# Optimization experiments

Hardware: AMD Instinct MI355X
Metric: run time of the kernel (lower is better)

The kernel has to match this reference:

```python
import jax, jax.numpy as jnp
import numpy as np
from jax.tree_util import tree_map

B, T, D = 2, 4096, 1024
C = 512            # chunk_size
P = 16             # n_persistent
H = 2048           # neural-memory hidden
FFN = 4 * D        # ffn_mult * d_model
LR, BETA, ALPHA = 0.01, 0.9, 0.01   # memory lr / momentum / decay
EPS_LN = 1e-5


def _l2norm(x):
    n = jnp.sqrt(jnp.sum(x * x, axis=-1, keepdims=True))
    return x / jnp.maximum(n, 1e-12)


def _ln(x, g, b):
    m = jnp.mean(x, axis=-1, keepdims=True)
    v = jnp.mean((x - m) ** 2, axis=-1, keepdims=True)
    return (x - m) * jax.lax.rsqrt(v + EPS_LN) * g + b


def _mem_mlp(mem, x):
    h = jax.nn.silu(x @ mem['w0'] + mem['b0'])
    return h @ mem['w1'] + mem['b1']


def setup_inputs() -> dict:
    key = jax.random.key(0)
    ks = iter(jax.random.split(key, 32))
    w = lambda *s: jax.random.normal(next(ks), s, jnp.float32) * 0.02
    return dict(
        x=jax.random.normal(next(ks), (B, T, D), jnp.float32),
        wq_ctx=w(D, D), wq=w(D, D), wk=w(D, D), wv=w(D, D),
        w_attn_out=w(D, D), w_gate=w(D, D),
        gate_g=jnp.ones(D), gate_b=jnp.zeros(D),
        n1_g=jnp.ones(D), n1_b=jnp.zeros(D),
        n2_g=jnp.ones(D), n2_b=jnp.zeros(D),
        ffn_w1=w(D, FFN), ffn_b1=jnp.zeros(FFN),
        ffn_w2=w(FFN, D), ffn_b2=jnp.zeros(D),
        pers=w(P, D),
        mem_w0=w(D, H), mem_b0=jnp.zeros(H),
        mem_w1=w(H, D), mem_b1=jnp.zeros(D),
        mem_wk=w(D, D), mem_wv=w(D, D),
    )


def reference(x, wq_ctx, wq, wk, wv, w_attn_out, w_gate, gate_g, gate_b,
              n1_g, n1_b, n2_g, n2_b, ffn_w1, ffn_b1, ffn_w2, ffn_b2,
              pers, mem_w0, mem_b0, mem_w1, mem_b1, mem_wk, mem_wv):
    Bv, Tv, Dv = x.shape
    n_chunks = Tv // C
    scale = Dv ** 0.5
    S = P + 2 * C   # persistent + retrieved-memory tokens + segment
    # prefix-aware causal mask: i attends to j if j < P (persistent prefix) or j <= i
    ii = jnp.arange(S)[:, None]
    jj = jnp.arange(S)[None, :]
    mask = (jj < P) | (jj <= ii)                      # (S, S)

    mem0 = dict(w0=mem_w0, b0=mem_b0, w1=mem_w1, b1=mem_b1)
    mom0 = tree_map(jnp.zeros_like, mem0)

    def attn(seq):                                    # cosine causal attention, single head
        q = _l2norm(seq @ wq) * scale
        k = _l2norm(seq @ wk)
        v = seq @ wv
        scores = jnp.einsum('bqd,bkd->bqk', q, k)
        scores = jnp.where(mask, scores, -jnp.inf)
        a = jax.nn.softmax(scores, axis=-1)
        return jnp.einsum('bqk,bkd->bqd', a, v) @ w_attn_out

    def step(carry, seg):                             # seg: (B, C, D)
        mem, mom = carry
        h = _mem_mlp(mem, _l2norm(seg @ wq_ctx))      # memory retrieval, (B, C, D)
        aug = jnp.concatenate(
            [jnp.broadcast_to(pers, (Bv, P, Dv)), h, seg], axis=1)  # (B, S, D)
        y_aug = aug + attn(_ln(aug, n1_g, n1_b))
        y_t = y_aug[:, P + C:, :]                     # strip persistent, keep last C

        # surprise-gradient memory update with momentum + decay
        kk = y_t @ mem_wk
        vv = y_t @ mem_wv
        loss = lambda m: 0.5 * jnp.sum((_mem_mlp(m, kk) - vv) ** 2) / (Bv * C)
        g = jax.grad(loss)(mem)
        mom = tree_map(lambda m_, g_: BETA * m_ + g_, mom, g)
        mem = tree_map(lambda p_, m_: (1.0 - ALPHA) * p_ - LR * m_, mem, mom)

        mem_out = _mem_mlp(mem, _l2norm(y_t @ wq_ctx))
        gate = jax.nn.sigmoid(_ln(y_t, gate_g, gate_b) @ w_gate)
        o = y_t * gate + mem_out * (1.0 - gate)
        h2 = _ln(o, n2_g, n2_b)
        o = o + (jax.nn.silu(h2 @ ffn_w1 + ffn_b1) @ ffn_w2 + ffn_b2)
        return (mem, mom), o

    x_chunks = x.reshape(Bv, n_chunks, C, Dv).transpose(1, 0, 2, 3)
    _, outs = jax.lax.scan(step, (mem0, mom0), x_chunks)   # (n_chunks, B, C, D)
    return outs.transpose(1, 0, 2, 3).reshape(Bv, Tv, Dv)
```

## Files before the change

kernel.cpp:

```cpp
#include <hip/hip_runtime.h>

#define DD 1024
#define HH 2048
#define TT 4096
#define CC 512
#define PPc 16
#define SB 1040
#define KA 1088
#define FFd 4096
#define NCH 8

typedef _Float16 f16x8 __attribute__((ext_vector_type(8)));
typedef float f32x4 __attribute__((ext_vector_type(4)));

typedef const __attribute__((address_space(1))) _Float16* gas_t;
typedef __attribute__((address_space(3))) _Float16* las_t;

__device__ __forceinline__ void async_cp16(const _Float16* g, _Float16* l) {
    __builtin_amdgcn_global_load_lds((gas_t)g, (las_t)l, 16, 0, 0);
}

template<int N> __device__ __forceinline__ void waitvm() {
    static_assert(N == 0 || N == 2 || N == 3 || N == 4 || N == 6 || N == 8, "unsupported vmcnt");
    if constexpr (N == 0)      asm volatile("s_waitcnt vmcnt(0)" ::: "memory");
    else if constexpr (N == 2) asm volatile("s_waitcnt vmcnt(2)" ::: "memory");
    else if constexpr (N == 3) asm volatile("s_waitcnt vmcnt(3)" ::: "memory");
    else if constexpr (N == 4) asm volatile("s_waitcnt vmcnt(4)" ::: "memory");
    else if constexpr (N == 6) asm volatile("s_waitcnt vmcnt(6)" ::: "memory");
    else                       asm volatile("s_waitcnt vmcnt(8)" ::: "memory");
}
#define BARRIER() asm volatile("s_barrier" ::: "memory")

struct GP {
    const _Float16* A; long bsA;
    const _Float16* Bt; long bsB;
    const float* bias;
    const float* resid; long ldr, bsR;
    const float* aux;   long ldx, bsX;
    float* Cf; long ldc, bsC;
    _Float16* Ch; long ldh, bsH;
    _Float16* Ct; long ldt, bsT;
    float* Mom;
    float* Cf2;
    float s1, s2;
    int M, N, K, act;
};

template<int BM, int BN>
__global__ __launch_bounds__(256) void gemm16(GP g)
{
    constexpr int WM = BM / 2, WN = BN / 2;
    constexpr int FA = WM / 16, FB = WN / 16;
    constexpr int LA = BM / 64, LB = BN / 64;
    constexpr int LL = LA + LB;
    constexpr int APAN = BM * 32, BPAN = BN * 32;
    __shared__ _Float16 smem[4 * (APAN + BPAN)];
    const int tid = threadIdx.x;

    const int gx = gridDim.x, gy = gridDim.y;
    const int nwg = gx * gy * (int)gridDim.z;
    const int orig = ((int)blockIdx.z * gy + (int)blockIdx.y) * gx + (int)blockIdx.x;
    const int xcd = orig & 7, loc = orig >> 3;
    const int q8 = nwg >> 3, r8 = nwg & 7;
    const int lid = (xcd < r8 ? xcd * (q8 + 1) : r8 * (q8 + 1) + (xcd - r8) * q8) + loc;
    const int bxi = lid % gx;
    const int rem = lid / gx;
    const int byi = rem % gy;
    const int z = rem / gy;

    const int K = g.K;
    const int m0 = byi * BM, n0 = bxi * BN;
    const _Float16* Ab = g.A + (long)z * g.bsA + (long)m0 * K;
    const _Float16* Bb = g.Bt + (long)z * g.bsB + (long)n0 * K;
    const int wave = tid >> 6, lane = tid & 63;
    const int wr = wave >> 1, wc = wave & 1;
    const int fr = lane & 15, kq = lane >> 4;
    const int srow = tid >> 2;
    const int scol = (tid & 3) * 8;
    f32x4 acc[FA][FB] = {};

    auto stage = [&](int q, int kk) {
#pragma unroll
        for (int r = 0; r < LA; ++r)
            async_cp16(Ab + (long)(r * 64 + srow) * K + kk + scol,
                       &smem[q * APAN + r * 2048 + wave * 512]);
#pragma unroll
        for (int r = 0; r < LB; ++r)
            async_cp16(Bb + (long)(r * 64 + srow) * K + kk + scol,
                       &smem[4 * APAN + q * BPAN + r * 2048 + wave * 512]);
    };

    auto compute = [&](int q) {
        f16x8 af[FA], bf[FB];
        const int ab = q * APAN + (wr * WM + fr) * 32 + kq * 8;
#pragma unroll
        for (int i = 0; i < FA; ++i) af[i] = *(const f16x8*)&smem[ab + i * 512];
        const int bb = 4 * APAN + q * BPAN + (wc * WN + fr) * 32 + kq * 8;
#pragma unroll
        for (int j = 0; j < FB; ++j) bf[j] = *(const f16x8*)&smem[bb + j * 512];
#pragma unroll
        for (int i = 0; i < FA; ++i)
#pragma unroll
            for (int j = 0; j < FB; ++j)
                acc[i][j] = __builtin_amdgcn_mfma_f32_16x16x32_f16(af[i], bf[j], acc[i][j], 0, 0, 0);
    };

    const int nk = K >> 5;
    stage(0, 0); stage(1, 32); stage(2, 64);
    for (int t = 0; t < nk - 2; ++t) {
        waitvm<2 * LL>();
        BARRIER();
        if (t + 3 < nk) stage((t + 3) & 3, (t + 3) << 5);
        compute(t & 3);
    }
    waitvm<LL>(); BARRIER(); compute((nk - 2) & 3);
    waitvm<0>();  BARRIER(); compute((nk - 1) & 3);

#pragma unroll
    for (int i = 0; i < FA; ++i) {
        const int gm0 = m0 + wr * WM + i * 16 + kq * 4;
#pragma unroll
        for (int j = 0; j < FB; ++j) {
            const int gn = n0 + wc * WN + j * 16 + fr;
            if (gn >= g.N) continue;
            if (g.act == 3) {
#pragma unroll
                for (int r = 0; r < 4; ++r) {
                    const int gm = gm0 + r;
                    if (gm >= g.M) continue;
                    const long idx = (long)gm * g.ldc + gn;
                    const float m = 0.9f * g.Mom[idx] + acc[i][j][r];
                    g.Mom[idx] = m;
                    const float v = 0.99f * g.Cf[idx] - 0.01f * m;
                    g.Cf[idx] = v;
                    if (g.Ch) g.Ch[(long)gm * g.ldh + gn] = (_Float16)v;
                    acc[i][j][r] = v;
                }
            } else if (g.act == 4) {
                const int seg = gn >> 10, gl = gn & 1023;
#pragma unroll
                for (int r = 0; r < 4; ++r) {
                    const int gm = gm0 + r;
                    if (gm >= g.M) continue;
                    const float v = acc[i][j][r];
                    if (seg == 0) g.Ch[(long)gm * 1024 + gl] = (_Float16)v;
                    else if (seg == 1) g.Cf[(long)gm * 1024 + gl] = v;
                    else g.Cf2[(long)gm * 1024 + gl] = v;
                }
            } else {
                const float bv = g.bias ? g.bias[gn] : 0.f;
#pragma unroll
                for (int r = 0; r < 4; ++r) {
                    const int gm = gm0 + r;
                    if (gm >= g.M) continue;
                    const float raw = acc[i][j][r] + bv;
                    float av = raw;
                    if (g.act == 1) av = raw / (1.f + __expf(-raw));
                    else if (g.act == 2) {
                        const float a = g.aux[(long)z * g.bsX + (long)gm * g.ldx + gn];
                        const float s = 1.f / (1.f + __expf(-a));
                        av = raw * (s * (1.f + a * (1.f - s)));
                    }
                    float v = g.s1 * av;
                    if (g.resid) v += g.s2 * g.resid[(long)z * g.bsR + (long)gm * g.ldr + gn];
                    if (g.Cf) g.Cf[(long)z * g.bsC + (long)gm * g.ldc + gn] = (g.act == 1) ? raw : v;
                    if (g.Ch) g.Ch[(long)z * g.bsH + (long)gm * g.ldh + gn] = (_Float16)v;
                    acc[i][j][r] = v;
                }
            }
        }
    }

    if (g.Ct && (g.act != 4 || n0 < 1024)) {
        constexpr int TP = BM + 8;
        __syncthreads();
#pragma unroll
        for (int i = 0; i < FA; ++i) {
            const int lm = wr * WM + i * 16 + kq * 4;
#pragma unroll
            for (int j = 0; j < FB; ++j) {
                const int ln = wc * WN + j * 16 + fr;
#pragma unroll
                for (int r = 0; r < 4; ++r)
                    smem[ln * TP + lm + r] = (_Float16)acc[i][j][r];
            }
        }
        __syncthreads();
        constexpr int TPC = 256 / BN;
        constexpr int SEG = BM / TPC;
        const int ln = tid / TPC, part = tid % TPC;
        const int gn = n0 + ln;
        if (gn < g.N) {
            const int gmb = m0 + part * SEG;
            _Float16* dst = g.Ct + (long)z * g.bsT + (long)gn * g.ldt + gmb;
            const _Float16* src = &smem[ln * TP + part * SEG];
#pragma unroll
            for (int gi = 0; gi < SEG / 8; ++gi)
                if (gmb + gi * 8 < g.M)
                    *(uint4*)(dst + gi * 8) = *(const uint4*)(src + gi * 8);
        }
    }
}

__global__ void cvt_k(const float* __restrict__ in, _Float16* __restrict__ out, long n)
{
    long i = ((long)blockIdx.x * 256 + threadIdx.x) * 4;
    if (i >= n) return;
    const float4 v = *(const float4*)(in + i);
    out[i] = (_Float16)v.x; out[i + 1] = (_Float16)v.y;
    out[i + 2] = (_Float16)v.z; out[i + 3] = (_Float16)v.w;
}

__global__ void cvtT_k(const float* __restrict__ in, _Float16* __restrict__ out, int R, int C)
{
    __shared__ _Float16 t[64][65];
    const int c0 = blockIdx.x * 64, r0 = blockIdx.y * 64;
    const int tid = threadIdx.x;
    for (int i = 0; i < 16; ++i) {
        const int lin = i * 256 + tid;
        const int r = lin >> 6, cc = lin & 63;
        t[r][cc] = (_Float16)in[(long)(r0 + r) * C + c0 + cc];
    }
    __syncthreads();
    for (int i = 0; i < 16; ++i) {
        const int lin = i * 256 + tid;
        const int r2 = lin >> 6, c2 = lin & 63;
        out[(long)(c0 + r2) * R + r0 + c2] = t[c2][r2];
    }
}

__global__ void l2n16s_k(const float* __restrict__ in, long ld,
                         _Float16* __restrict__ out, float scale)
{
    const long row = blockIdx.x;
    const float* p = in + row * ld;
    _Float16* q = out + row * DD;
    const int t = threadIdx.x;
    float e0 = p[t], e1 = p[t + 256], e2 = p[t + 512], e3 = p[t + 768];
    __shared__ float rq[256];
    rq[t] = e0 * e0 + e1 * e1 + e2 * e2 + e3 * e3;
    __syncthreads();
    for (int k = 128; k; k >>= 1) { if (t < k) rq[t] += rq[t + k]; __syncthreads(); }
    const float f = scale / fmaxf(sqrtf(rq[0]), 1e-12f);
    q[t] = (_Float16)(e0 * f); q[t + 256] = (_Float16)(e1 * f);
    q[t + 512] = (_Float16)(e2 * f); q[t + 768] = (_Float16)(e3 * f);
}

__global__ void l2qk_k(const float* __restrict__ qk, _Float16* __restrict__ q16,
                       _Float16* __restrict__ k16)
{
    const int blk = blockIdx.x;
    const float* p; _Float16* o; float scale;
    if (blk < 1024) {
        const int b = blk >> 9, r = blk & 511;
        p = qk + (long)(b * SB + PPc + CC + r) * 2048;
        o = q16 + (long)blk * DD; scale = 32.f;
    } else {
        const int row = blk - 1024;
        p = qk + (long)row * 2048 + 1024;
        o = k16 + (long)row * DD; scale = 1.f;
    }
    const int t = threadIdx.x;
    float e0 = p[t], e1 = p[t + 256], e2 = p[t + 512], e3 = p[t + 768];
    __shared__ float rq[256];
    rq[t] = e0 * e0 + e1 * e1 + e2 * e2 + e3 * e3;
    __syncthreads();
    for (int k = 128; k; k >>= 1) { if (t < k) rq[t] += rq[t + k]; __syncthreads(); }
    const float f = scale / fmaxf(sqrtf(rq[0]), 1e-12f);
    o[t] = (_Float16)(e0 * f); o[t + 256] = (_Float16)(e1 * f);
    o[t + 512] = (_Float16)(e2 * f); o[t + 768] = (_Float16)(e3 * f);
}

__global__ void ln16_k(const float* __restrict__ x, const float* __restrict__ g,
                       const float* __restrict__ b, _Float16* __restrict__ o)
{
    const long row = blockIdx.x;
    const float* p = x + row * DD;
    _Float16* q = o + row * DD;
    const int t = threadIdx.x;
    float e0 = p[t], e1 = p[t + 256], e2 = p[t + 512], e3 = p[t + 768];
    __shared__ float rs[256], rq[256];
    rs[t] = e0 + e1 + e2 + e3;
    rq[t] = e0 * e0 + e1 * e1 + e2 * e2 + e3 * e3;
    __syncthreads();
    for (int k = 128; k; k >>= 1) {
        if (t < k) { rs[t] += rs[t + k]; rq[t] += rq[t + k]; }
        __syncthreads();
    }
    const float mean = rs[0] * (1.f / DD);
    const float inv = rsqrtf(rq[0] * (1.f / DD) - mean * mean + 1e-5f);
    q[t]       = (_Float16)((e0 - mean) * inv * g[t]       + b[t]);
    q[t + 256] = (_Float16)((e1 - mean) * inv * g[t + 256] + b[t + 256]);
    q[t + 512] = (_Float16)((e2 - mean) * inv * g[t + 512] + b[t + 512]);
    q[t + 768] = (_Float16)((e3 - mean) * inv * g[t + 768] + b[t + 768]);
}

__global__ void lnaug_k(const float* __restrict__ x, const float* __restrict__ pers,
                        const float* __restrict__ h, const float* __restrict__ g,
                        const float* __restrict__ b, _Float16* __restrict__ out, int c)
{
    const int row = blockIdx.x;
    const int bb = row / SB, i = row % SB;
    const float* p;
    if (i < PPc) p = pers + (long)i * DD;
    else if (i < PPc + CC) p = h + (long)(bb * CC + i - PPc) * DD;
    else p = x + (long)(bb * TT + c * CC + (i - PPc - CC)) * DD;
    _Float16* q = out + (long)row * DD;
    const int t = threadIdx.x;
    float e0 = p[t], e1 = p[t + 256], e2 = p[t + 512], e3 = p[t + 768];
    __shared__ float rs[256], rq[256];
    rs[t] = e0 + e1 + e2 + e3;
    rq[t] = e0 * e0 + e1 * e1 + e2 * e2 + e3 * e3;
    __syncthreads();
    for (int k = 128; k; k >>= 1) {
        if (t < k) { rs[t] += rs[t + k]; rq[t] += rq[t + k]; }
        __syncthreads();
    }
    const float mean = rs[0] * (1.f / DD);
    const float inv = rsqrtf(rq[0] * (1.f / DD) - mean * mean + 1e-5f);
    q[t]       = (_Float16)((e0 - mean) * inv * g[t]       + b[t]);
    q[t + 256] = (_Float16)((e1 - mean) * inv * g[t + 256] + b[t + 256]);
    q[t + 512] = (_Float16)((e2 - mean) * inv * g[t + 512] + b[t + 512]);
    q[t + 768] = (_Float16)((e3 - mean) * inv * g[t + 768] + b[t + 768]);
}

__global__ void softmax16_k(const float* __restrict__ sc, _Float16* __restrict__ pr)
{
    const int blk = blockIdx.x;
    const int r = blk & 511;
    const int i = PPc + CC + r;
    const float* p = sc + (long)blk * SB;
    _Float16* q = pr + (long)blk * KA;
    const int t = threadIdx.x;
    __shared__ float red[256];
    float mx = -3.0e38f;
    for (int j = t; j < SB; j += 256)
        if (j <= i) mx = fmaxf(mx, p[j]);
    red[t] = mx; __syncthreads();
    for (int k = 128; k; k >>= 1) { if (t < k) red[t] = fmaxf(red[t], red[t + k]); __syncthreads(); }
    mx = red[0]; __syncthreads();
    float sum = 0.f;
    for (int j = t; j < SB; j += 256)
        if (j <= i) sum += __expf(p[j] - mx);
    red[t] = sum; __syncthreads();
    for (int k = 128; k; k >>= 1) { if (t < k) red[t] += red[t + k]; __syncthreads(); }
    const float inv = 1.f / red[0];
    for (int j = t; j < KA; j += 256) {
        float e = 0.f;
        if (j < SB && j <= i) e = __expf(p[j] - mx) * inv;
        q[j] = (_Float16)e;
    }
}

__global__ void gateln2_k(const float* __restrict__ yt, const float* __restrict__ gp,
                          const float* __restrict__ mo, const float* __restrict__ g,
                          const float* __restrict__ b, float* __restrict__ OF,
                          _Float16* __restrict__ o16)
{
    const long row = blockIdx.x;
    const int t = threadIdx.x;
    float e[4];
    __shared__ float rs[256], rq[256];
    float ssum = 0.f, qsum = 0.f;
#pragma unroll
    for (int k = 0; k < 4; ++k) {
        const long idx = row * DD + t + k * 256;
        const float s = 1.f / (1.f + __expf(-gp[idx]));
        e[k] = yt[idx] * s + mo[idx] * (1.f - s);
        OF[idx] = e[k];
        ssum += e[k]; qsum += e[k] * e[k];
    }
    rs[t] = ssum; rq[t] = qsum;
    __syncthreads();
    for (int k = 128; k; k >>= 1) {
        if (t < k) { rs[t] += rs[t + k]; rq[t] += rq[t + k]; }
        __syncthreads();
    }
    const float mean = rs[0] * (1.f / DD);
    const float inv = rsqrtf(rq[0] * (1.f / DD) - mean * mean + 1e-5f);
#pragma unroll
    for (int k = 0; k < 4; ++k) {
        const int cc = t + k * 256;
        o16[row * DD + cc] = (_Float16)((e[k] - mean) * inv * g[cc] + b[cc]);
    }
}

__global__ void rowsum2_k(const _Float16* __restrict__ rT, const _Float16* __restrict__ daT,
                          float* __restrict__ db1, float* __restrict__ db0)
{
    const int blk = blockIdx.x;
    const _Float16* p; float* o;
    if (blk < 1024) { p = rT + (long)blk * 1024; o = db1 + blk; }
    else { p = daT + (long)(blk - 1024) * 1024; o = db0 + (blk - 1024); }
    const int t = threadIdx.x;
    __shared__ float red[256];
    red[t] = (float)p[t] + (float)p[t + 256] + (float)p[t + 512] + (float)p[t + 768];
    __syncthreads();
    for (int k = 128; k; k >>= 1) { if (t < k) red[t] += red[t + k]; __syncthreads(); }
    if (t == 0) *o = red[0];
}

__global__ void biasup_k(float* __restrict__ mb0, float* __restrict__ mob0,
                         const float* __restrict__ db0,
                         float* __restrict__ mb1, float* __restrict__ mob1,
                         const float* __restrict__ db1)
{
    const int i = blockIdx.x * 256 + threadIdx.x;
    if (i < HH) {
        const float m = 0.9f * mob0[i] + db0[i];
        mob0[i] = m;
        mb0[i] = 0.99f * mb0[i] - 0.01f * m;
    } else {
        const int j = i - HH;
        if (j < DD) {
            const float m = 0.9f * mob1[j] + db1[j];
            mob1[j] = m;
            mb1[j] = 0.99f * mb1[j] - 0.01f * m;
        }
    }
}

__global__ void zero_k(float* __restrict__ p, long n)
{
    long i = (long)blockIdx.x * 256 + threadIdx.x;
    const long st = (long)gridDim.x * 256;
    for (; i < n; i += st) p[i] = 0.f;
}

extern "C" void kernel_launch(void* const* d_in, const int* in_sizes, int n_in,
                              void* d_out, int out_size, void* d_ws, size_t ws_size,
                              hipStream_t stream)
{
    const float* x          = (const float*)d_in[0];
    const float* wq_ctx     = (const float*)d_in[1];
    const float* wq         = (const float*)d_in[2];
    const float* wk         = (const float*)d_in[3];
    const float* wv         = (const float*)d_in[4];
    const float* w_attn_out = (const float*)d_in[5];
    const float* w_gate     = (const float*)d_in[6];
    const float* gate_g     = (const float*)d_in[7];
    const float* gate_b     = (const float*)d_in[8];
    const float* n1_g       = (const float*)d_in[9];
    const float* n1_b       = (const float*)d_in[10];
    const float* n2_g       = (const float*)d_in[11];
    const float* n2_b       = (const float*)d_in[12];
    const float* ffn_w1     = (const float*)d_in[13];
    const float* ffn_b1     = (const float*)d_in[14];
    const float* ffn_w2     = (const float*)d_in[15];
    const float* ffn_b2     = (const float*)d_in[16];
    const float* pers       = (const float*)d_in[17];
    const float* mem_w0_in  = (const float*)d_in[18];
    const float* mem_b0_in  = (const float*)d_in[19];
    const float* mem_w1_in  = (const float*)d_in[20];
    const float* mem_b1_in  = (const float*)d_in[21];
    const float* mem_wk     = (const float*)d_in[22];
    const float* mem_wv     = (const float*)d_in[23];
    float* out = (float*)d_out;
    (void)in_sizes; (void)n_in; (void)out_size; (void)ws_size;

    char* cur = (char*)d_ws;
    auto allocF = [&](size_t n) { float* p = (float*)cur; cur += n * 4; return p; };
    auto allocH = [&](size_t n) { _Float16* p = (_Float16*)cur; cur += n * 2; return p; };

    float* mw0   = allocF((size_t)DD * HH);
    float* mw1   = allocF((size_t)HH * DD);
    float* mb0   = allocF(HH);
    float* mb1   = allocF(DD);
    float* mom   = allocF((size_t)DD * HH * 2 + HH + DD);
    float* mom_w0 = mom, *mom_w1 = mom + (size_t)DD * HH;
    float* mom_b0 = mom_w1 + (size_t)HH * DD, *mom_b1 = mom_b0 + HH;
    float* F32A  = allocF((size_t)1024 * DD);
    float* F32B  = allocF((size_t)1024 * DD);
    float* F32C  = allocF((size_t)1024 * HH);
    float* F32QK = allocF((size_t)2112 * 2048);
    float* YTF   = allocF((size_t)1024 * DD);
    float* OF    = allocF((size_t)1024 * DD);
    float* db0   = allocF(HH);
    float* db1   = allocF(DD);

    _Float16* x16    = allocH((size_t)2 * TT * DD);
    _Float16* wqcT   = allocH((size_t)DD * DD);
    _Float16* wqkT   = allocH((size_t)2048 * DD);
    _Float16* wvT    = allocH((size_t)DD * DD);
    _Float16* waoT   = allocH((size_t)DD * DD);
    _Float16* wgT    = allocH((size_t)DD * DD);
    _Float16* wmixT  = allocH((size_t)3072 * DD);
    _Float16* f1T    = allocH((size_t)FFd * DD);
    _Float16* f2T    = allocH((size_t)DD * FFd);
    _Float16* w0T    = allocH((size_t)HH * DD);
    _Float16* w1T    = allocH((size_t)DD * HH);
    _Float16* w1p    = allocH((size_t)HH * DD);
    _Float16* xn16   = allocH((size_t)1024 * DD);
    _Float16* h116   = allocH((size_t)1024 * HH);
    _Float16* laug16 = allocH((size_t)2208 * DD);
    _Float16* q16    = allocH((size_t)1024 * DD);
    _Float16* k16    = allocH((size_t)2208 * DD);
    _Float16* vT16   = allocH((size_t)2 * DD * KA);
    _Float16* pr16   = allocH((size_t)2 * 512 * KA);
    _Float16* ao16   = allocH((size_t)1024 * DD);
    _Float16* yt16   = allocH((size_t)1024 * DD);
    _Float16* kk16   = allocH((size_t)1024 * DD);
    _Float16* kkT16  = allocH((size_t)DD * 1024);
    _Float16* hs16   = allocH((size_t)1024 * HH);
    _Float16* hsT16  = allocH((size_t)HH * 1024);
    _Float16* r16    = allocH((size_t)1024 * DD);
    _Float16* rT16   = allocH((size_t)DD * 1024);
    _Float16* da0T   = allocH((size_t)HH * 1024);
    _Float16* qm16   = allocH((size_t)1024 * DD);
    _Float16* a216   = allocH((size_t)1024 * HH);
    _Float16* gl16   = allocH((size_t)1024 * DD);
    _Float16* h216   = allocH((size_t)1024 * DD);
    _Float16* f116   = allocH((size_t)1024 * FFd);

    auto launch = [&](int bm, int bn, int nz, const GP& g) {
        dim3 grid((g.N + bn - 1) / bn, (g.M + bm - 1) / bm, nz);
        if (bm == 128)     gemm16<128, 128><<<grid, 256, 0, stream>>>(g);
        else if (bn == 128) gemm16<64, 128><<<grid, 256, 0, stream>>>(g);
        else                gemm16<64, 64><<<grid, 256, 0, stream>>>(g);
    };

    hipMemcpyAsync(mw0, mem_w0_in, sizeof(float) * DD * HH, hipMemcpyDeviceToDevice, stream);
    hipMemcpyAsync(mw1, mem_w1_in, sizeof(float) * HH * DD, hipMemcpyDeviceToDevice, stream);
    hipMemcpyAsync(mb0, mem_b0_in, sizeof(float) * HH, hipMemcpyDeviceToDevice, stream);
    hipMemcpyAsync(mb1, mem_b1_in, sizeof(float) * DD, hipMemcpyDeviceToDevice, stream);
    zero_k<<<4096, 256, 0, stream>>>(mom, (long)DD * HH * 2 + HH + DD);
    cvt_k<<<(2 * TT * DD) / 1024, 256, 0, stream>>>(x, x16, (long)2 * TT * DD);
    auto T64 = [&](const float* in, _Float16* o, int R, int C) {
        cvtT_k<<<dim3(C / 64, R / 64), 256, 0, stream>>>(in, o, R, C);
    };
    T64(wq_ctx, wqcT, DD, DD);
    T64(wq, wqkT, DD, DD); T64(wk, wqkT + (size_t)1024 * DD, DD, DD);
    T64(wv, wvT, DD, DD); T64(w_attn_out, waoT, DD, DD); T64(w_gate, wgT, DD, DD);
    T64(mem_wk, wmixT, DD, DD); T64(mem_wv, wmixT + (size_t)1024 * DD, DD, DD);
    T64(wq_ctx, wmixT + (size_t)2048 * DD, DD, DD);
    T64(ffn_w1, f1T, DD, FFd); T64(ffn_w2, f2T, FFd, DD);
    T64(mem_w0_in, w0T, DD, HH); T64(mem_w1_in, w1T, HH, DD);
    cvt_k<<<(HH * DD) / 1024, 256, 0, stream>>>(mem_w1_in, w1p, (long)HH * DD);

    for (int c = 0; c < NCH; ++c) {
        GP g;
        g = GP{}; g.A = x16 + (long)c * CC * DD; g.bsA = (long)TT * DD; g.Bt = wqcT;
        g.Cf = F32A; g.ldc = DD; g.bsC = (long)CC * DD;
        g.s1 = 1.f; g.M = CC; g.N = DD; g.K = DD;
        launch(64, 64, 2, g);
        l2n16s_k<<<1024, 256, 0, stream>>>(F32A, DD, xn16, 1.f);
        g = GP{}; g.A = xn16; g.Bt = w0T; g.bias = mb0; g.Ch = h116; g.ldh = HH;
        g.s1 = 1.f; g.M = 1024; g.N = HH; g.K = DD; g.act = 1;
        launch(64, 128, 1, g);
        g = GP{}; g.A = h116; g.Bt = w1T; g.bias = mb1; g.Cf = F32B; g.ldc = DD;
        g.s1 = 1.f; g.M = 1024; g.N = DD; g.K = HH;
        launch(64, 64, 1, g);
        lnaug_k<<<2 * SB, 256, 0, stream>>>(x, pers, F32B, n1_g, n1_b, laug16, c);
        g = GP{}; g.A = laug16; g.Bt = wqkT; g.Cf = F32QK; g.ldc = 2048;
        g.s1 = 1.f; g.M = 2 * SB; g.N = 2048; g.K = DD;
        launch(64, 128, 1, g);
        l2qk_k<<<3104, 256, 0, stream>>>(F32QK, q16, k16);
        g = GP{}; g.A = laug16; g.bsA = (long)SB * DD; g.Bt = wvT;
        g.Ct = vT16; g.ldt = KA; g.bsT = (long)DD * KA;
        g.s1 = 1.f; g.M = SB; g.N = DD; g.K = DD;
        launch(64, 64, 2, g);
        g = GP{}; g.A = q16; g.bsA = (long)512 * DD; g.Bt = k16; g.bsB = (long)SB * DD;
        g.Cf = F32C; g.ldc = SB; g.bsC = (long)512 * SB;
        g.s1 = 1.f; g.M = 512; g.N = SB; g.K = DD;
        launch(64, 64, 2, g);
        softmax16_k<<<1024, 256, 0, stream>>>(F32C, pr16);
        g = GP{}; g.A = pr16; g.bsA = (long)512 * KA; g.Bt = vT16; g.bsB = (long)DD * KA;
        g.Ch = ao16; g.ldh = DD; g.bsH = (long)512 * DD;
        g.s1 = 1.f; g.M = 512; g.N = DD; g.K = KA;
        launch(64, 64, 2, g);
        g = GP{}; g.A = ao16; g.bsA = (long)512 * DD; g.Bt = waoT;
        g.resid = x + (long)c * CC * DD; g.ldr = DD; g.bsR = (long)TT * DD;
        g.Cf = YTF; g.ldc = DD; g.bsC = (long)512 * DD;
        g.Ch = yt16; g.ldh = DD; g.bsH = (long)512 * DD;
        g.s1 = 1.f; g.s2 = 1.f; g.M = 512; g.N = DD; g.K = DD;
        launch(64, 64, 2, g);
        g = GP{}; g.A = yt16; g.Bt = wmixT; g.Ch = kk16; g.Ct = kkT16; g.ldt = 1024;
        g.Cf = F32B; g.Cf2 = F32A;
        g.s1 = 1.f; g.M = 1024; g.N = 3072; g.K = DD; g.act = 4;
        launch(64, 128, 1, g);
        g = GP{}; g.A = kk16; g.Bt = w0T; g.bias = mb0; g.Cf = F32C; g.ldc = HH;
        g.Ch = hs16; g.ldh = HH; g.Ct = hsT16; g.ldt = 1024;
        g.s1 = 1.f; g.M = 1024; g.N = HH; g.K = DD; g.act = 1;
        launch(64, 128, 1, g);
        g = GP{}; g.A = hs16; g.Bt = w1T; g.bias = mb1;
        g.resid = F32B; g.ldr = DD;
        g.Ch = r16; g.ldh = DD; g.Ct = rT16; g.ldt = 1024;
        g.s1 = 1.f / 1024.f; g.s2 = -1.f / 1024.f; g.M = 1024; g.N = DD; g.K = HH;
        launch(64, 64, 1, g);
        g = GP{}; g.A = r16; g.Bt = w1p; g.aux = F32C; g.ldx = HH;
        g.Ct = da0T; g.ldt = 1024;
        g.s1 = 1.f; g.M = 1024; g.N = HH; g.K = DD; g.act = 2;
        launch(64, 128, 1, g);
        rowsum2_k<<<3072, 256, 0, stream>>>(rT16, da0T, db1, db0);
        g = GP{}; g.A = hsT16; g.Bt = rT16; g.Cf = mw1; g.ldc = DD; g.Mom = mom_w1;
        g.Ch = w1p; g.ldh = DD; g.Ct = w1T; g.ldt = HH;
        g.M = HH; g.N = DD; g.K = 1024; g.act = 3;
        launch(64, 64, 1, g);
        g = GP{}; g.A = kkT16; g.Bt = da0T; g.Cf = mw0; g.ldc = HH; g.Mom = mom_w0;
        g.Ct = w0T; g.ldt = DD;
        g.M = DD; g.N = HH; g.K = 1024; g.act = 3;
        launch(64, 128, 1, g);
        biasup_k<<<12, 256, 0, stream>>>(mb0, mom_b0, db0, mb1, mom_b1, db1);
        l2n16s_k<<<1024, 256, 0, stream>>>(F32A, DD, qm16, 1.f);
        g = GP{}; g.A = qm16; g.Bt = w0T; g.bias = mb0; g.Ch = a216; g.ldh = HH;
        g.s1 = 1.f; g.M = 1024; g.N = HH; g.K = DD; g.act = 1;
        launch(64, 128, 1, g);
        g = GP{}; g.A = a216; g.Bt = w1T; g.bias = mb1; g.Cf = F32B; g.ldc = DD;
        g.s1 = 1.f; g.M = 1024; g.N = DD; g.K = HH;
        launch(64, 64, 1, g);
        ln16_k<<<1024, 256, 0, stream>>>(YTF, gate_g, gate_b, gl16);
        g = GP{}; g.A = gl16; g.Bt = wgT; g.Cf = F32C; g.ldc = DD;
        g.s1 = 1.f; g.M = 1024; g.N = DD; g.K = DD;
        launch(64, 64, 1, g);
        gateln2_k<<<1024, 256, 0, stream>>>(YTF, F32C, F32B, n2_g, n2_b, OF, h216);
        g = GP{}; g.A = h216; g.Bt = f1T; g.bias = ffn_b1; g.Ch = f116; g.ldh = FFd;
        g.s1 = 1.f; g.M = 1024; g.N = FFd; g.K = DD; g.act = 1;
        launch(128, 128, 1, g);
        g = GP{}; g.A = f116; g.bsA = (long)512 * FFd; g.Bt = f2T; g.bias = ffn_b2;
        g.resid = OF; g.ldr = DD; g.bsR = (long)512 * DD;
        g.Cf = out + (long)c * CC * DD; g.ldc = DD; g.bsC = (long)TT * DD;
        g.s1 = 1.f; g.s2 = 1.f; g.M = 512; g.N = DD; g.K = FFd;
        launch(64, 64, 2, g);
    }
}
```

Before: 3.575 ms.

## Deepen GEMM K-tile to 64 with XOR-swizzled LDS and triple buffering

The shared GEMM kernel now stages K-tiles of 64 instead of 32. It uses an XOR swizzle on LDS columns to avoid bank conflicts, and a 3-stage ring buffer instead of 4 stages. MFMA issue is wrapped in s_setprio, and all launches use the 64x64 tile instead of choosing 64x128 or 128x128 per GEMM. This halves the number of barriers per K loop and reduces LDS conflicts, but the larger FFN GEMMs now launch many more small tiles and lose data reuse.

```diff
diff --git a/kernel.cpp b/kernel.cpp
--- a/kernel.cpp
+++ b/kernel.cpp
@@ -51,10 +51,11 @@
 {
     constexpr int WM = BM / 2, WN = BN / 2;
     constexpr int FA = WM / 16, FB = WN / 16;
-    constexpr int LA = BM / 64, LB = BN / 64;
+    constexpr int LA = BM / 32, LB = BN / 32;
     constexpr int LL = LA + LB;
-    constexpr int APAN = BM * 32, BPAN = BN * 32;
-    __shared__ _Float16 smem[4 * (APAN + BPAN)];
+    constexpr int APAN = BM * 64, BPAN = BN * 64;
+    constexpr int NB = 3;
+    __shared__ _Float16 smem[NB * (APAN + BPAN)];
     const int tid = threadIdx.x;
 
     const int gx = gridDim.x, gy = gridDim.y;
@@ -75,46 +76,62 @@
     const int wave = tid >> 6, lane = tid & 63;
     const int wr = wave >> 1, wc = wave & 1;
     const int fr = lane & 15, kq = lane >> 4;
-    const int srow = tid >> 2;
-    const int scol = (tid & 3) * 8;
+    const int srow = tid >> 3;
+    const int sc8 = (((tid & 7) ^ (srow & 7)) << 3);
     f32x4 acc[FA][FB] = {};
 
     auto stage = [&](int q, int kk) {
 #pragma unroll
         for (int r = 0; r < LA; ++r)
-            async_cp16(Ab + (long)(r * 64 + srow) * K + kk + scol,
+            async_cp16(Ab + (long)(r * 32 + srow) * K + kk + sc8,
                        &smem[q * APAN + r * 2048 + wave * 512]);
 #pragma unroll
         for (int r = 0; r < LB; ++r)
-            async_cp16(Bb + (long)(r * 64 + srow) * K + kk + scol,
-                       &smem[4 * APAN + q * BPAN + r * 2048 + wave * 512]);
+            async_cp16(Bb + (long)(r * 32 + srow) * K + kk + sc8,
+                       &smem[NB * APAN + q * BPAN + r * 2048 + wave * 512]);
     };
 
+    const int sl0 = ((kq ^ (fr & 7)) << 3);
+    const int sl1 = (((4 + kq) ^ (fr & 7)) << 3);
+
     auto compute = [&](int q) {
-        f16x8 af[FA], bf[FB];
-        const int ab = q * APAN + (wr * WM + fr) * 32 + kq * 8;
-#pragma unroll
-        for (int i = 0; i < FA; ++i) af[i] = *(const f16x8*)&smem[ab + i * 512];
-        const int bb = 4 * APAN + q * BPAN + (wc * WN + fr) * 32 + kq * 8;
-#pragma unroll
-        for (int j = 0; j < FB; ++j) bf[j] = *(const f16x8*)&smem[bb + j * 512];
-#pragma unroll
-        for (int i = 0; i < FA; ++i)
-#pragma unroll
-            for (int j = 0; j < FB; ++j)
-                acc[i][j] = __builtin_amdgcn_mfma_f32_16x16x32_f16(af[i], bf[j], acc[i][j], 0, 0, 0);
+        f16x8 af[2][FA], bf[2][FB];
+        const int abase = q * APAN;
+#pragma unroll
+        for (int i = 0; i < FA; ++i) {
+            const int ro = (wr * WM + i * 16 + fr) * 64;
+            af[0][i] = *(const f16x8*)&smem[abase + ro + sl0];
+            af[1][i] = *(const f16x8*)&smem[abase + ro + sl1];
+        }
+        const int bbase = NB * APAN + q * BPAN;
+#pragma unroll
+        for (int j = 0; j < FB; ++j) {
+            const int ro = (wc * WN + j * 16 + fr) * 64;
+            bf[0][j] = *(const f16x8*)&smem[bbase + ro + sl0];
+            bf[1][j] = *(const f16x8*)&smem[bbase + ro + sl1];
+        }
+        __builtin_amdgcn_s_setprio(1);
+#pragma unroll
+        for (int h = 0; h < 2; ++h)
+#pragma unroll
+            for (int i = 0; i < FA; ++i)
+#pragma unroll
+                for (int j = 0; j < FB; ++j)
+                    acc[i][j] = __builtin_amdgcn_mfma_f32_16x16x32_f16(af[h][i], bf[h][j], acc[i][j], 0, 0, 0);
+        __builtin_amdgcn_s_setprio(0);
     };
 
-    const int nk = K >> 5;
-    stage(0, 0); stage(1, 32); stage(2, 64);
-    for (int t = 0; t < nk - 2; ++t) {
-        waitvm<2 * LL>();
+    const int nk = K >> 6;
+    stage(0, 0); stage(1, 64);
+    int qc = 0, qs = 2;
+    for (int t = 0; t < nk; ++t) {
+        if (t + 1 < nk) waitvm<LL>(); else waitvm<0>();
         BARRIER();
-        if (t + 3 < nk) stage((t + 3) & 3, (t + 3) << 5);
-        compute(t & 3);
-    }
-    waitvm<LL>(); BARRIER(); compute((nk - 2) & 3);
-    waitvm<0>();  BARRIER(); compute((nk - 1) & 3);
+        if (t + 2 < nk) stage(qs, (t + 2) << 6);
+        compute(qc);
+        qc = (qc == NB - 1) ? 0 : qc + 1;
+        qs = (qs == NB - 1) ? 0 : qs + 1;
+    }
 
 #pragma unroll
     for (int i = 0; i < FA; ++i) {
@@ -512,11 +529,9 @@
     _Float16* h216   = allocH((size_t)1024 * DD);
     _Float16* f116   = allocH((size_t)1024 * FFd);
 
-    auto launch = [&](int bm, int bn, int nz, const GP& g) {
-        dim3 grid((g.N + bn - 1) / bn, (g.M + bm - 1) / bm, nz);
-        if (bm == 128)     gemm16<128, 128><<<grid, 256, 0, stream>>>(g);
-        else if (bn == 128) gemm16<64, 128><<<grid, 256, 0, stream>>>(g);
-        else                gemm16<64, 64><<<grid, 256, 0, stream>>>(g);
+    auto launch = [&](int nz, const GP& g) {
+        dim3 grid((g.N + 63) / 64, (g.M + 63) / 64, nz);
+        gemm16<64, 64><<<grid, 256, 0, stream>>>(g);
     };
 
     hipMemcpyAsync(mw0, mem_w0_in, sizeof(float) * DD * HH, hipMemcpyDeviceToDevice, stream);
@@ -542,84 +557,84 @@
         g = GP{}; g.A = x16 + (long)c * CC * DD; g.bsA = (long)TT * DD; g.Bt = wqcT;
         g.Cf = F32A; g.ldc = DD; g.bsC = (long)CC * DD;
         g.s1 = 1.f; g.M = CC; g.N = DD; g.K = DD;
-        launch(64, 64, 2, g);
+        launch(2, g);
         l2n16s_k<<<1024, 256, 0, stream>>>(F32A, DD, xn16, 1.f);
         g = GP{}; g.A = xn16; g.Bt = w0T; g.bias = mb0; g.Ch = h116; g.ldh = HH;
         g.s1 = 1.f; g.M = 1024; g.N = HH; g.K = DD; g.act = 1;
-        launch(64, 128, 1, g);
+        launch(1, g);
         g = GP{}; g.A = h116; g.Bt = w1T; g.bias = mb1; g.Cf = F32B; g.ldc = DD;
         g.s1 = 1.f; g.M = 1024; g.N = DD; g.K = HH;
-        launch(64, 64, 1, g);
+        launch(1, g);
         lnaug_k<<<2 * SB, 256, 0, stream>>>(x, pers, F32B, n1_g, n1_b, laug16, c);
         g = GP{}; g.A = laug16; g.Bt = wqkT; g.Cf = F32QK; g.ldc = 2048;
         g.s1 = 1.f; g.M = 2 * SB; g.N = 2048; g.K = DD;
-        launch(64, 128, 1, g);
+        launch(1, g);
         l2qk_k<<<3104, 256, 0, stream>>>(F32QK, q16, k16);
         g = GP{}; g.A = laug16; g.bsA = (long)SB * DD; g.Bt = wvT;
         g.Ct = vT16; g.ldt = KA; g.bsT = (long)DD * KA;
         g.s1 = 1.f; g.M = SB; g.N = DD; g.K = DD;
-        launch(64, 64, 2, g);
+        launch(2, g);
         g = GP{}; g.A = q16; g.bsA = (long)512 * DD; g.Bt = k16; g.bsB = (long)SB * DD;
         g.Cf = F32C; g.ldc = SB; g.bsC = (long)512 * SB;
         g.s1 = 1.f; g.M = 512; g.N = SB; g.K = DD;
-        launch(64, 64, 2, g);
+        launch(2, g);
         softmax16_k<<<1024, 256, 0, stream>>>(F32C, pr16);
         g = GP{}; g.A = pr16; g.bsA = (long)512 * KA; g.Bt = vT16; g.bsB = (long)DD * KA;
         g.Ch = ao16; g.ldh = DD; g.bsH = (long)512 * DD;
         g.s1 = 1.f; g.M = 512; g.N = DD; g.K = KA;
-        launch(64, 64, 2, g);
+        launch(2, g);
         g = GP{}; g.A = ao16; g.bsA = (long)512 * DD; g.Bt = waoT;
         g.resid = x + (long)c * CC * DD; g.ldr = DD; g.bsR = (long)TT * DD;
         g.Cf = YTF; g.ldc = DD; g.bsC = (long)512 * DD;
         g.Ch = yt16; g.ldh = DD; g.bsH = (long)512 * DD;
         g.s1 = 1.f; g.s2 = 1.f; g.M = 512; g.N = DD; g.K = DD;
-        launch(64, 64, 2, g);
+        launch(2, g);
         g = GP{}; g.A = yt16; g.Bt = wmixT; g.Ch = kk16; g.Ct = kkT16; g.ldt = 1024;
         g.Cf = F32B; g.Cf2 = F32A;
         g.s1 = 1.f; g.M = 1024; g.N = 3072; g.K = DD; g.act = 4;
-        launch(64, 128, 1, g);
+        launch(1, g);
         g = GP{}; g.A = kk16; g.Bt = w0T; g.bias = mb0; g.Cf = F32C; g.ldc = HH;
         g.Ch = hs16; g.ldh = HH; g.Ct = hsT16; g.ldt = 1024;
         g.s1 = 1.f; g.M = 1024; g.N = HH; g.K = DD; g.act = 1;
-        launch(64, 128, 1, g);
+        launch(1, g);
         g = GP{}; g.A = hs16; g.Bt = w1T; g.bias = mb1;
         g.resid = F32B; g.ldr = DD;
         g.Ch = r16; g.ldh = DD; g.Ct = rT16; g.ldt = 1024;
         g.s1 = 1.f / 1024.f; g.s2 = -1.f / 1024.f; g.M = 1024; g.N = DD; g.K = HH;
-        launch(64, 64, 1, g);
+        launch(1, g);
         g = GP{}; g.A = r16; g.Bt = w1p; g.aux = F32C; g.ldx = HH;
         g.Ct = da0T; g.ldt = 1024;
         g.s1 = 1.f; g.M = 1024; g.N = HH; g.K = DD; g.act = 2;
-        launch(64, 128, 1, g);
+        launch(1, g);
         rowsum2_k<<<3072, 256, 0, stream>>>(rT16, da0T, db1, db0);
         g = GP{}; g.A = hsT16; g.Bt = rT16; g.Cf = mw1; g.ldc = DD; g.Mom = mom_w1;
         g.Ch = w1p; g.ldh = DD; g.Ct = w1T; g.ldt = HH;
         g.M = HH; g.N = DD; g.K = 1024; g.act = 3;
-        launch(64, 64, 1, g);
+        launch(1, g);
         g = GP{}; g.A = kkT16; g.Bt = da0T; g.Cf = mw0; g.ldc = HH; g.Mom = mom_w0;
         g.Ct = w0T; g.ldt = DD;
         g.M = DD; g.N = HH; g.K = 1024; g.act = 3;
-        launch(64, 128, 1, g);
+        launch(1, g);
         biasup_k<<<12, 256, 0, stream>>>(mb0, mom_b0, db0, mb1, mom_b1, db1);
         l2n16s_k<<<1024, 256, 0, stream>>>(F32A, DD, qm16, 1.f);
         g = GP{}; g.A = qm16; g.Bt = w0T; g.bias = mb0; g.Ch = a216; g.ldh = HH;
         g.s1 = 1.f; g.M = 1024; g.N = HH; g.K = DD; g.act = 1;
-        launch(64, 128, 1, g);
+        launch(1, g);
         g = GP{}; g.A = a216; g.Bt = w1T; g.bias = mb1; g.Cf = F32B; g.ldc = DD;
         g.s1 = 1.f; g.M = 1024; g.N = DD; g.K = HH;
-        launch(64, 64, 1, g);
+        launch(1, g);
         ln16_k<<<1024, 256, 0, stream>>>(YTF, gate_g, gate_b, gl16);
         g = GP{}; g.A = gl16; g.Bt = wgT; g.Cf = F32C; g.ldc = DD;
         g.s1 = 1.f; g.M = 1024; g.N = DD; g.K = DD;
-        launch(64, 64, 1, g);
+        launch(1, g);
         gateln2_k<<<1024, 256, 0, stream>>>(YTF, F32C, F32B, n2_g, n2_b, OF, h216);
         g = GP{}; g.A = h216; g.Bt = f1T; g.bias = ffn_b1; g.Ch = f116; g.ldh = FFd;
         g.s1 = 1.f; g.M = 1024; g.N = FFd; g.K = DD; g.act = 1;
-        launch(128, 128, 1, g);
+        launch(1, g);
         g = GP{}; g.A = f116; g.bsA = (long)512 * FFd; g.Bt = f2T; g.bias = ffn_b2;
         g.resid = OF; g.ldr = DD; g.bsR = (long)512 * DD;
         g.Cf = out + (long)c * CC * DD; g.ldc = DD; g.bsC = (long)TT * DD;
         g.s1 = 1.f; g.s2 = 1.f; g.M = 512; g.N = DD; g.K = FFd;
-        launch(64, 64, 2, g);
-    }
-}
+        launch(2, g);
+    }
+}
```

After: 3.152 ms. -11.8%, faster.
